# Kernel tuning notes

Hardware: AMD Instinct MI355X
Metric: run time of the kernel (lower is better)

Reference implementation:

```python
import jax, jax.numpy as jnp
import numpy as np

NHEAD = 16
EPS_ATTN = 1e-6
EPS_LN = 1e-5


def _layer_norm(x, g, b):
    mu = jnp.mean(x, -1, keepdims=True)
    var = jnp.mean((x - mu) ** 2, -1, keepdims=True)
    return (x - mu) * jax.lax.rsqrt(var + EPS_LN) * g + b


def _run_layer(x, S_prev, z_prev, lp, m):
    # x: (B,E); S_prev: (B,H,D,D); z_prev: (B,H,D,1); m: (B,1,1) or None
    qkv_w, qkv_b, out_w, out_b, n1g, n1b, n2g, n2b, f1w, f1b, f2w, f2b = lp
    B, E = x.shape
    H = NHEAD
    D = E // H
    qkv = x @ qkv_w.T + qkv_b
    q, k, v = [t.reshape(B, H, D) for t in jnp.split(qkv, 3, -1)]
    q = jax.nn.elu(q) + 1.0
    k = jax.nn.elu(k) + 1.0
    if m is not None:
        k = k * m
        v = v * m
    S_new = S_prev + jnp.einsum('bhd,bhm->bhdm', k, v)
    z_new = z_prev + k[..., None]
    num = jnp.einsum('bhd,bhdm->bhm', q, S_new)
    den = jnp.einsum('bhd,bhd->bh', q, z_new[..., 0])[..., None]
    attn = (num / (den + EPS_ATTN)).reshape(B, E)
    x = _layer_norm(x + attn @ out_w.T + out_b, n1g, n1b)
    h = jax.nn.relu(x @ f1w.T + f1b) @ f2w.T + f2b
    x = _layer_norm(x + h, n2g, n2b)
    return x, S_new, z_new


def _scan_layers(x_t, Ss, zs, params, m):
    # params: tuple of arrays each with leading layer dim L
    def body(x, xs):
        lp, S, z = xs
        x, S, z = _run_layer(x, S, z, lp, m)
        return x, (S, z)
    x_out, (Ss_new, zs_new) = jax.lax.scan(body, x_t, (params, Ss, zs))
    return x_out, Ss_new, zs_new


def _forward(x, lengths, out_lengths, emb_w, emb_b, enc_p, dec_p, fc_p):
    B, Slen, _ = x.shape
    E = emb_w.shape[0]
    H = NHEAD
    D = E // H
    L = enc_p[0].shape[0]
    h = x @ emb_w.T + emb_b
    # sinusoidal positional encoding
    pos = jnp.arange(Slen, dtype=h.dtype)[:, None]
    div = jnp.exp(jnp.arange(0, E, 2, dtype=h.dtype) * (-np.log(10000.0) / E))
    pe = jnp.zeros((Slen, E), h.dtype)
    pe = pe.at[:, 0::2].set(jnp.sin(pos * div)).at[:, 1::2].set(jnp.cos(pos * div))
    h = h + pe[None]
    mask = (jnp.arange(Slen)[None, :] < lengths[:, None]).astype(h.dtype)  # (B,S)
    Ss0 = jnp.zeros((L, B, H, D, D), h.dtype)
    zs0 = jnp.zeros((L, B, H, D, 1), h.dtype)

    def enc_step(carry, inp):
        Ss, zs, _ = carry
        x_t, m_t = inp
        x_out, Ss, zs = _scan_layers(x_t, Ss, zs, enc_p, m_t[:, None, None])
        return (Ss, zs, x_out), None

    (Ss, zs, x_last), _ = jax.lax.scan(
        enc_step, (Ss0, zs0, jnp.zeros((B, E), h.dtype)),
        (h.transpose(1, 0, 2), mask.T))

    fc1_w, fc1_b, fc2_w, fc2_b = fc_p

    def dec_step(carry, _):
        xd, Ss, zs = carry
        xd, Ss, zs = _scan_layers(xd, Ss, zs, dec_p, None)
        out = jax.nn.relu(xd @ fc1_w.T + fc1_b) @ fc2_w.T + fc2_b
        return (xd, Ss, zs), out

    _, outs = jax.lax.scan(dec_step, (x_last, Ss, zs), None, length=out_lengths)
    return outs.transpose(1, 0, 2)  # (B, out_lengths, num_classes)


def setup_inputs() -> dict:
    key = jax.random.key(0)
    B, S, IN, E, L, C, TOUT = 4, 256, 256, 1024, 4, 1000, 32
    ks = iter(jax.random.split(key, 64))

    def w(shape, s=0.02):
        return jax.random.normal(next(ks), shape, jnp.float32) * s

    d = {}
    d['x'] = jax.random.normal(next(ks), (B, S, IN), jnp.float32)
    d['lengths'] = jax.random.randint(next(ks), (B,), 1, S + 1)
    d['out_lengths'] = TOUT
    d['emb_w'] = w((E, IN))
    d['emb_b'] = jnp.zeros((E,), jnp.float32)
    for pre in ('enc', 'dec'):
        d[f'{pre}_qkv_w'] = w((L, 3 * E, E))
        d[f'{pre}_qkv_b'] = jnp.zeros((L, 3 * E), jnp.float32)
        d[f'{pre}_out_w'] = w((L, E, E))
        d[f'{pre}_out_b'] = jnp.zeros((L, E), jnp.float32)
        d[f'{pre}_n1g'] = jnp.ones((L, E), jnp.float32)
        d[f'{pre}_n1b'] = jnp.zeros((L, E), jnp.float32)
        d[f'{pre}_n2g'] = jnp.ones((L, E), jnp.float32)
        d[f'{pre}_n2b'] = jnp.zeros((L, E), jnp.float32)
        d[f'{pre}_f1w'] = w((L, E, E))  # dim_feedforward == hidden_size
        d[f'{pre}_f1b'] = jnp.zeros((L, E), jnp.float32)
        d[f'{pre}_f2w'] = w((L, E, E))
        d[f'{pre}_f2b'] = jnp.zeros((L, E), jnp.float32)
    d['fc1_w'] = w((E, E))
    d['fc1_b'] = jnp.zeros((E,), jnp.float32)
    d['fc2_w'] = w((C, E))
    d['fc2_b'] = jnp.zeros((C,), jnp.float32)
    return d


def reference(x, lengths, out_lengths, emb_w, emb_b,
              enc_qkv_w, enc_qkv_b, enc_out_w, enc_out_b, enc_n1g, enc_n1b,
              enc_n2g, enc_n2b, enc_f1w, enc_f1b, enc_f2w, enc_f2b,
              dec_qkv_w, dec_qkv_b, dec_out_w, dec_out_b, dec_n1g, dec_n1b,
              dec_n2g, dec_n2b, dec_f1w, dec_f1b, dec_f2w, dec_f2b,
              fc1_w, fc1_b, fc2_w, fc2_b):
    enc_p = (enc_qkv_w, enc_qkv_b, enc_out_w, enc_out_b, enc_n1g, enc_n1b,
             enc_n2g, enc_n2b, enc_f1w, enc_f1b, enc_f2w, enc_f2b)
    dec_p = (dec_qkv_w, dec_qkv_b, dec_out_w, dec_out_b, dec_n1g, dec_n1b,
             dec_n2g, dec_n2b, dec_f1w, dec_f1b, dec_f2w, dec_f2b)
    fc_p = (fc1_w, fc1_b, fc2_w, fc2_b)
    return _forward(x, lengths, out_lengths, emb_w, emb_b, enc_p, dec_p, fc_p)
```

## Files before the change

### kernel.cpp

```cpp
#include <hip/hip_runtime.h>
#include <hip/hip_bf16.h>
#include <cstdint>


#define EP_NONE     0
#define EP_PE       1
#define EP_QKV      2
#define EP_RELU     3
#define EP_RES      4

typedef __attribute__((ext_vector_type(8))) short bf8v;
typedef __attribute__((ext_vector_type(8))) unsigned short us8;
typedef __attribute__((ext_vector_type(4))) float f4_t;

__device__ __forceinline__ float bf2f(unsigned short s) {
    union { unsigned u; float f; } t; t.u = ((unsigned)s) << 16; return t.f;
}
__device__ __forceinline__ unsigned short f2bf(float f) {
    union { float f; unsigned u; } t; t.f = f;
    unsigned u = t.u;
    unsigned r = u + 0x7FFFu + ((u >> 16) & 1u);
    return (unsigned short)(r >> 16);
}
__device__ __forceinline__ float ldS(const void* p, size_t i, bool b) {
    return b ? bf2f(((const unsigned short*)p)[i]) : ((const float*)p)[i];
}
__device__ __forceinline__ void ld4d(const void* p, size_t i, bool b, float o[4]) {
    if (b) {
        ushort4 v = *(const ushort4*)((const unsigned short*)p + i);
        o[0] = bf2f(v.x); o[1] = bf2f(v.y); o[2] = bf2f(v.z); o[3] = bf2f(v.w);
    } else {
        float4 v = *(const float4*)((const float*)p + i);
        o[0] = v.x; o[1] = v.y; o[2] = v.z; o[3] = v.w;
    }
}
__device__ __forceinline__ void stS(void* p, size_t i, bool b, float v) {
    if (b) ((unsigned short*)p)[i] = f2bf(v);
    else   ((float*)p)[i] = v;
}

__device__ __forceinline__ void split_store(unsigned short* hp, unsigned short* lp,
                                            const float fv[8]) {
    us8 h, l;
#pragma unroll
    for (int i = 0; i < 8; ++i) {
        unsigned short hh = f2bf(fv[i]);
        h[i] = (short)hh;
        l[i] = f2bf(fv[i] - bf2f(hh));
    }
    *(us8*)hp = h;
    *(us8*)lp = l;
}

__global__ void detect_k(const unsigned* __restrict__ ones,
                         const int* __restrict__ lens, int* __restrict__ flag)
{
    if (threadIdx.x == 0 && blockIdx.x == 0) {
        flag[0] = (ones[0] == 0x3F803F80u) ? 1 : 0;
        flag[1] = (lens[1] == 0 && lens[3] == 0) ? 1 : 0;
    }
}

template <int EPI>
__global__ __launch_bounds__(256) void mgemm_k(
    const void* __restrict__ A, int a_ext, int t0, int chb,
    const void* __restrict__ W, size_t woff,
    const void* __restrict__ bias, size_t boff,
    const float* __restrict__ res, float* __restrict__ C,
    int M, int N, int K,
    const int* __restrict__ lengths, const int* __restrict__ flag)
{
    (void)M;
    const bool ebf = flag[0] != 0;
    const bool abf = ebf && (a_ext != 0);
    __shared__ __align__(16) unsigned short Ah[64][40];
    __shared__ __align__(16) unsigned short Al[64][40];
    __shared__ __align__(16) unsigned short Bh[64][40];
    __shared__ __align__(16) unsigned short Bl[64][40];

    const int tid = threadIdx.x;
    const int n0 = blockIdx.x << 6, m0 = blockIdx.y << 6;
    const int chm = (1 << chb) - 1;

    const int srow = tid >> 2;
    const int sc0 = (tid & 3) << 3;
    const int lrowA = m0 + srow;
    const size_t arow = a_ext ? ((size_t)(lrowA >> chb) * 256 + t0 + (lrowA & chm))
                              : (size_t)lrowA;
    const size_t abase = arow * (size_t)K + sc0;
    const size_t wbase = woff + (size_t)(n0 + srow) * K + sc0;

    const int lane = tid & 63;
    const int wv4 = tid >> 6;
    const int wm = (wv4 >> 1) << 5;
    const int wn = (wv4 & 1) << 5;
    const int fr = lane & 15;
    const int fk = (lane >> 4) << 3;

    f4_t a00 = {}, a01 = {}, a10 = {}, a11 = {};

    for (int k0 = 0; k0 < K; k0 += 32) {
        if (abf) {
            const unsigned short* ap = (const unsigned short*)A + abase + k0;
            *(us8*)&Ah[srow][sc0] = *(const us8*)ap;
            us8 z = {};
            *(us8*)&Al[srow][sc0] = z;
        } else {
            const float* ap = (const float*)A + abase + k0;
            float4 f0 = *(const float4*)ap;
            float4 f1 = *(const float4*)(ap + 4);
            float fv[8] = {f0.x, f0.y, f0.z, f0.w, f1.x, f1.y, f1.z, f1.w};
            split_store(&Ah[srow][sc0], &Al[srow][sc0], fv);
        }
        if (ebf) {
            const unsigned short* wp = (const unsigned short*)W + wbase + k0;
            *(us8*)&Bh[srow][sc0] = *(const us8*)wp;
        } else {
            const float* wp = (const float*)W + wbase + k0;
            float4 f0 = *(const float4*)wp;
            float4 f1 = *(const float4*)(wp + 4);
            float fv[8] = {f0.x, f0.y, f0.z, f0.w, f1.x, f1.y, f1.z, f1.w};
            split_store(&Bh[srow][sc0], &Bl[srow][sc0], fv);
        }
        __syncthreads();

        bf8v ah0 = *(const bf8v*)&Ah[wm + fr][fk];
        bf8v ah1 = *(const bf8v*)&Ah[wm + 16 + fr][fk];
        bf8v bh0 = *(const bf8v*)&Bh[wn + fr][fk];
        bf8v bh1 = *(const bf8v*)&Bh[wn + 16 + fr][fk];
        a00 = __builtin_amdgcn_mfma_f32_16x16x32_bf16(ah0, bh0, a00, 0, 0, 0);
        a01 = __builtin_amdgcn_mfma_f32_16x16x32_bf16(ah0, bh1, a01, 0, 0, 0);
        a10 = __builtin_amdgcn_mfma_f32_16x16x32_bf16(ah1, bh0, a10, 0, 0, 0);
        a11 = __builtin_amdgcn_mfma_f32_16x16x32_bf16(ah1, bh1, a11, 0, 0, 0);
        if (!abf) {
            bf8v al0 = *(const bf8v*)&Al[wm + fr][fk];
            bf8v al1 = *(const bf8v*)&Al[wm + 16 + fr][fk];
            a00 = __builtin_amdgcn_mfma_f32_16x16x32_bf16(al0, bh0, a00, 0, 0, 0);
            a01 = __builtin_amdgcn_mfma_f32_16x16x32_bf16(al0, bh1, a01, 0, 0, 0);
            a10 = __builtin_amdgcn_mfma_f32_16x16x32_bf16(al1, bh0, a10, 0, 0, 0);
            a11 = __builtin_amdgcn_mfma_f32_16x16x32_bf16(al1, bh1, a11, 0, 0, 0);
        }
        if (!ebf) {
            bf8v bl0 = *(const bf8v*)&Bl[wn + fr][fk];
            bf8v bl1 = *(const bf8v*)&Bl[wn + 16 + fr][fk];
            a00 = __builtin_amdgcn_mfma_f32_16x16x32_bf16(ah0, bl0, a00, 0, 0, 0);
            a01 = __builtin_amdgcn_mfma_f32_16x16x32_bf16(ah0, bl1, a01, 0, 0, 0);
            a10 = __builtin_amdgcn_mfma_f32_16x16x32_bf16(ah1, bl0, a10, 0, 0, 0);
            a11 = __builtin_amdgcn_mfma_f32_16x16x32_bf16(ah1, bl1, a11, 0, 0, 0);
        }
        __syncthreads();
    }

    f4_t accs[2][2] = {{a00, a01}, {a10, a11}};
    const int rb = m0 + wm + ((lane >> 4) << 2);
    const int cb = n0 + wn + fr;
#pragma unroll
    for (int i = 0; i < 2; ++i) {
#pragma unroll
        for (int e = 0; e < 4; ++e) {
            const int r = rb + i * 16 + e;
#pragma unroll
            for (int j = 0; j < 2; ++j) {
                const int c = cb + j * 16;
                float v = accs[i][j][e] + ldS(bias, boff + c, ebf);
                if constexpr (EPI == EP_PE) {
                    int t = t0 + (r & chm);
                    float freq = expf((float)(c & ~1) * (-9.210340371976184f / 1024.0f));
                    float ang = (float)t * freq;
                    v += (c & 1) ? cosf(ang) : sinf(ang);
                } else if constexpr (EPI == EP_QKV) {
                    if (c < 2048)
                        v = v > 0.f ? v + 1.f : expf(v);
                    if (c >= 1024) {
                        int bb = r >> chb, t = t0 + (r & chm);
                        int len = lengths[flag[1] ? (bb << 1) : bb];
                        if (t >= len) v = 0.f;
                    }
                } else if constexpr (EPI == EP_RELU) {
                    v = fmaxf(v, 0.f);
                } else if constexpr (EPI == EP_RES) {
                    v += res[(size_t)r * N + c];
                }
                C[(size_t)r * N + c] = v;
            }
        }
    }
}

__global__ __launch_bounds__(64) void enc_attn_k(
    const float* __restrict__ qkvc, float* __restrict__ attnc,
    float* __restrict__ Sst, float* __restrict__ zst, int first, int CH)
{
    const int bid = blockIdx.x;
    const int mg = bid & 3, h = (bid >> 2) & 15, b = bid >> 6;
    const int bh = b * 16 + h;
    const int tid = threadIdx.x;
    const int ml = tid & 15, d4 = tid >> 4, db = d4 << 4;
    const int m = (mg << 4) + ml;

    float Sa[16], za[16];
    if (first) {
#pragma unroll
        for (int j = 0; j < 16; ++j) { Sa[j] = 0.f; za[j] = 0.f; }
    } else {
#pragma unroll
        for (int j = 0; j < 16; ++j) {
            Sa[j] = Sst[(size_t)bh * 4096 + (size_t)(db + j) * 64 + m];
            za[j] = zst[(size_t)bh * 64 + db + j];
        }
    }

    __shared__ float ks[32][64];
    __shared__ float qs[32][64];
    __shared__ float vs[32][16];

    for (int s = 0; s < CH; s += 32) {
        __syncthreads();
        for (int r = 0; r < 32; ++r) {
            const float* p = qkvc + (size_t)(b * CH + s + r) * 3072 + (h << 6);
            qs[r][tid] = p[tid];
            ks[r][tid] = p[1024 + tid];
        }
        for (int i = tid; i < 512; i += 64) {
            int r = i >> 4, c = i & 15;
            vs[r][c] = qkvc[(size_t)(b * CH + s + r) * 3072 + 2048 + (h << 6) + (mg << 4) + c];
        }
        __syncthreads();

        for (int tt = 0; tt < 32; ++tt) {
            float v = vs[tt][ml];
            const float4* k4 = (const float4*)&ks[tt][db];
            const float4* q4 = (const float4*)&qs[tt][db];
            float pn = 0.f, pd = 0.f;
#pragma unroll
            for (int j = 0; j < 4; ++j) {
                float4 kk = k4[j], qq = q4[j];
                Sa[4*j+0] += kk.x * v; za[4*j+0] += kk.x;
                Sa[4*j+1] += kk.y * v; za[4*j+1] += kk.y;
                Sa[4*j+2] += kk.z * v; za[4*j+2] += kk.z;
                Sa[4*j+3] += kk.w * v; za[4*j+3] += kk.w;
                pn += qq.x*Sa[4*j+0] + qq.y*Sa[4*j+1] + qq.z*Sa[4*j+2] + qq.w*Sa[4*j+3];
                pd += qq.x*za[4*j+0] + qq.y*za[4*j+1] + qq.z*za[4*j+2] + qq.w*za[4*j+3];
            }
            pn += __shfl_xor(pn, 16); pd += __shfl_xor(pd, 16);
            pn += __shfl_xor(pn, 32); pd += __shfl_xor(pd, 32);
            if (d4 == 0)
                attnc[(size_t)(b * CH + s + tt) * 1024 + (h << 6) + m] = pn / (pd + 1e-6f);
        }
    }

#pragma unroll
    for (int j = 0; j < 16; ++j)
        Sst[(size_t)bh * 4096 + (size_t)(db + j) * 64 + m] = Sa[j];
    if (ml == 0) {
#pragma unroll
        for (int j = 0; j < 16; ++j)
            zst[(size_t)bh * 64 + db + j] = za[j];
    }
}

__global__ __launch_bounds__(256) void ln_k(
    float* __restrict__ Y, const void* __restrict__ g, size_t goff,
    const void* __restrict__ b, size_t boff, const int* __restrict__ flag)
{
    const bool ebf = flag[0] != 0;
    __shared__ float red[256];
    const int row = blockIdx.x, tid = threadIdx.x;
    float4* y4 = (float4*)(Y + (size_t)row * 1024);
    float4 x = y4[tid];
    red[tid] = x.x + x.y + x.z + x.w;
    __syncthreads();
    for (int o = 128; o > 0; o >>= 1) {
        if (tid < o) red[tid] += red[tid + o];
        __syncthreads();
    }
    float mu = red[0] * (1.0f / 1024.0f);
    __syncthreads();
    float dx = x.x - mu, dy = x.y - mu, dz = x.z - mu, dw = x.w - mu;
    red[tid] = dx * dx + dy * dy + dz * dz + dw * dw;
    __syncthreads();
    for (int o = 128; o > 0; o >>= 1) {
        if (tid < o) red[tid] += red[tid + o];
        __syncthreads();
    }
    float rs = rsqrtf(red[0] * (1.0f / 1024.0f) + 1e-5f);
    float gv[4], bv[4];
    ld4d(g, goff + (size_t)tid * 4, ebf, gv);
    ld4d(b, boff + (size_t)tid * 4, ebf, bv);
    float4 o;
    o.x = dx * rs * gv[0] + bv[0];
    o.y = dy * rs * gv[1] + bv[1];
    o.z = dz * rs * gv[2] + bv[2];
    o.w = dw * rs * gv[3] + bv[3];
    y4[tid] = o;
}

template <int EPI, bool XN, int RES, bool ODYN>
__global__ __launch_bounds__(256) void sgemm2_k(
    const float* __restrict__ x,
    const void* __restrict__ lxg, size_t lxgo,
    const void* __restrict__ lxb, size_t lxbo,
    const float* __restrict__ res,
    const void* __restrict__ lrg, size_t lrgo,
    const void* __restrict__ lrb, size_t lrbo,
    const void* __restrict__ W, size_t woff,
    const void* __restrict__ bias, size_t boff,
    void* __restrict__ C, int N, int K, int ldc, int coff,
    const int* __restrict__ flag)
{
    const bool ebf = flag[0] != 0;
    const int wv = threadIdx.x >> 6, lane = threadIdx.x & 63;
    __shared__ float sxm[4], sxr[4], srm[4], srr[4];

    if (XN) {
        const float4* xr = (const float4*)(x + (size_t)wv * K);
        float s = 0.f, q = 0.f;
        for (int i = lane; i < (K >> 2); i += 64) {
            float4 v = xr[i];
            s += v.x + v.y + v.z + v.w;
            q += v.x*v.x + v.y*v.y + v.z*v.z + v.w*v.w;
        }
        for (int o2 = 32; o2; o2 >>= 1) { s += __shfl_xor(s, o2); q += __shfl_xor(q, o2); }
        if (lane == 0) {
            float mu = s / (float)K;
            sxm[wv] = mu;
            sxr[wv] = rsqrtf(q / (float)K - mu * mu + 1e-5f);
        }
    }
    if (RES == 2) {
        const float4* rr = (const float4*)(res + (size_t)wv * N);
        float s = 0.f, q = 0.f;
        for (int i = lane; i < (N >> 2); i += 64) {
            float4 v = rr[i];
            s += v.x + v.y + v.z + v.w;
            q += v.x*v.x + v.y*v.y + v.z*v.z + v.w*v.w;
        }
        for (int o2 = 32; o2; o2 >>= 1) { s += __shfl_xor(s, o2); q += __shfl_xor(q, o2); }
        if (lane == 0) {
            float mu = s / (float)N;
            srm[wv] = mu;
            srr[wv] = rsqrtf(q / (float)N - mu * mu + 1e-5f);
        }
    }
    if (XN || RES == 2) __syncthreads();

    const int n = blockIdx.x * 4 + wv;
    const size_t wbase = woff + (size_t)n * K;
    const float4* x0 = (const float4*)(x);
    const float4* x1 = (const float4*)(x + K);
    const float4* x2 = (const float4*)(x + 2 * K);
    const float4* x3 = (const float4*)(x + 3 * K);
    float m0=0,r0=1,m1=0,r1=1,m2=0,r2=1,m3=0,r3=1;
    if (XN) {
        m0 = sxm[0]; r0 = sxr[0]; m1 = sxm[1]; r1 = sxr[1];
        m2 = sxm[2]; r2 = sxr[2]; m3 = sxm[3]; r3 = sxr[3];
    }
    float a0 = 0.f, a1 = 0.f, a2 = 0.f, a3 = 0.f;
    for (int i = lane; i < (K >> 2); i += 64) {
        float w[4];
        ld4d(W, wbase + (size_t)i * 4, ebf, w);
        float g[4], be[4];
        if (XN) {
            ld4d(lxg, lxgo + (size_t)i * 4, ebf, g);
            ld4d(lxb, lxbo + (size_t)i * 4, ebf, be);
        }
        float4 v;
#define ROWACC(XP, ACC, MU, RS)                                               \
        v = XP[i];                                                            \
        if (XN) {                                                             \
            ACC += ((v.x - MU) * RS * g[0] + be[0]) * w[0]                    \
                 + ((v.y - MU) * RS * g[1] + be[1]) * w[1]                    \
                 + ((v.z - MU) * RS * g[2] + be[2]) * w[2]                    \
                 + ((v.w - MU) * RS * g[3] + be[3]) * w[3];                   \
        } else {                                                              \
            ACC += v.x * w[0] + v.y * w[1] + v.z * w[2] + v.w * w[3];         \
        }
        ROWACC(x0, a0, m0, r0)
        ROWACC(x1, a1, m1, r1)
        ROWACC(x2, a2, m2, r2)
        ROWACC(x3, a3, m3, r3)
#undef ROWACC
    }
    for (int o2 = 32; o2; o2 >>= 1) {
        a0 += __shfl_down(a0, o2);
        a1 += __shfl_down(a1, o2);
        a2 += __shfl_down(a2, o2);
        a3 += __shfl_down(a3, o2);
    }
    if (lane == 0) {
        float bn = ldS(bias, boff + n, ebf);
        float v[4] = {a0 + bn, a1 + bn, a2 + bn, a3 + bn};
        float rg = 0.f, rb = 0.f;
        if (RES == 2) { rg = ldS(lrg, lrgo + n, ebf); rb = ldS(lrb, lrbo + n, ebf); }
#pragma unroll
        for (int b2 = 0; b2 < 4; ++b2) {
            if constexpr (RES == 1) {
                v[b2] += res[(size_t)b2 * N + n];
            } else if constexpr (RES == 2) {
                v[b2] += (res[(size_t)b2 * N + n] - srm[b2]) * srr[b2] * rg + rb;
            }
            if constexpr (EPI == EP_QKV) {
                if (n < 2048) v[b2] = v[b2] > 0.f ? v[b2] + 1.f : expf(v[b2]);
            } else if constexpr (EPI == EP_RELU) {
                v[b2] = fmaxf(v[b2], 0.f);
            }
            size_t idx = (size_t)coff + (size_t)b2 * ldc + n;
            if constexpr (ODYN) stS(C, idx, ebf, v[b2]);
            else                ((float*)C)[idx] = v[b2];
        }
    }
}

__global__ __launch_bounds__(64) void dec_attn_k(
    const float* __restrict__ qkv, float* __restrict__ Sst,
    float* __restrict__ zst, float* __restrict__ attn)
{
    const int bh = blockIdx.x;
    const int b = bh >> 4, h = bh & 15;
    const int lane = threadIdx.x;
    const float* base = qkv + (size_t)b * 3072 + (h << 6);
    float q = base[lane];
    float k = base[1024 + lane];
    float v = base[2048 + lane];
    __shared__ float kq[128];
    kq[lane] = k;
    kq[64 + lane] = q;
    float* zp = zst + (size_t)bh * 64;
    float zn = zp[lane] + k;
    zp[lane] = zn;
    float p = q * zn;
    for (int off = 32; off; off >>= 1) p += __shfl_xor(p, off);
    float den = p + 1e-6f;
    __syncthreads();
    float* Sp = Sst + (size_t)bh * 4096;
    float num = 0.f;
#pragma unroll 8
    for (int d = 0; d < 64; ++d) {
        float s = Sp[d * 64 + lane] + kq[d] * v;
        Sp[d * 64 + lane] = s;
        num += kq[64 + d] * s;
    }
    attn[(size_t)b * 1024 + (h << 6) + lane] = num / den;
}

__global__ __launch_bounds__(256) void copy_last_k(
    const float* __restrict__ Xc, float* __restrict__ xd, int CH)
{
    int i = blockIdx.x * 256 + threadIdx.x;
    int b = i >> 10, e = i & 1023;
    xd[i] = Xc[(size_t)(b * CH + CH - 1) * 1024 + e];
}

extern "C" void kernel_launch(void* const* d_in, const int* in_sizes, int n_in,
                              void* d_out, int out_size, void* d_ws, size_t ws_size,
                              hipStream_t stream)
{
    (void)n_in; (void)out_size;
    constexpr int E = 1024, B = 4, L = 4, TOUT = 32, NC = 1000;

    const int CH  = (ws_size >= (size_t)30 * 1024 * 1024) ? 256 : 32;
    const int chb = (CH == 256) ? 8 : 5;
    const int NCH = 256 / CH;
    const int MC  = B * CH;

    const int o = (in_sizes[2] == 1) ? 0 : -1;

    const void* x_in = d_in[0];
    const int*  lens = (const int*)d_in[1];
    const void* emb_w = d_in[3 + o];
    const void* emb_b = d_in[4 + o];
    const void* e_qkv_w = d_in[5 + o];  const void* e_qkv_b = d_in[6 + o];
    const void* e_out_w = d_in[7 + o];  const void* e_out_b = d_in[8 + o];
    const void* e_n1g = d_in[9 + o];    const void* e_n1b = d_in[10 + o];
    const void* e_n2g = d_in[11 + o];   const void* e_n2b = d_in[12 + o];
    const void* e_f1w = d_in[13 + o];   const void* e_f1b = d_in[14 + o];
    const void* e_f2w = d_in[15 + o];   const void* e_f2b = d_in[16 + o];
    const void* d_qkv_w = d_in[17 + o]; const void* d_qkv_b = d_in[18 + o];
    const void* d_out_w = d_in[19 + o]; const void* d_out_b = d_in[20 + o];
    const void* d_n1g = d_in[21 + o];   const void* d_n1b = d_in[22 + o];
    const void* d_n2g = d_in[23 + o];   const void* d_n2b = d_in[24 + o];
    const void* d_f1w = d_in[25 + o];   const void* d_f1b = d_in[26 + o];
    const void* d_f2w = d_in[27 + o];   const void* d_f2b = d_in[28 + o];
    const void* fc1_w = d_in[29 + o];   const void* fc1_b = d_in[30 + o];
    const void* fc2_w = d_in[31 + o];   const void* fc2_b = d_in[32 + o];

    float* wsf   = (float*)d_ws;
    int*   flag  = (int*)d_ws;
    float* u     = wsf + 64;
    float* t1    = u + B * E;
    float* qkvd  = t1 + B * E;
    float* attnd = qkvd + B * 3 * E;
    float* hfd   = attnd + B * E;
    float* Xc    = hfd + B * E;
    float* Yc    = Xc + (size_t)MC * E;
    float* attnc = Yc + (size_t)MC * E;
    float* qkvc  = attnc + (size_t)MC * E;
    float* zs    = qkvc + (size_t)MC * 3 * E;
    float* Ss    = zs + (size_t)L * B * 16 * 64;
    float* Hc    = qkvc;

    const size_t SstL = (size_t)B * 16 * 64 * 64;
    const size_t zstL = (size_t)B * 16 * 64;

    detect_k<<<1, 64, 0, stream>>>((const unsigned*)e_n1g, lens, flag);

    for (int c = 0; c < NCH; ++c) {
        const int t0 = c * CH;
        mgemm_k<EP_PE><<<dim3(E / 64, MC / 64), 256, 0, stream>>>(
            x_in, 1, t0, chb, emb_w, 0, emb_b, 0, nullptr, Xc,
            MC, E, 256, lens, flag);

        for (int l = 0; l < L; ++l) {
            const size_t qw_o = (size_t)l * 3 * E * E, qb_o = (size_t)l * 3 * E;
            const size_t ow_o = (size_t)l * E * E,     ob_o = (size_t)l * E;
            const size_t fw_o = (size_t)l * E * E,     fb_o = (size_t)l * E;
            const size_t g_o  = (size_t)l * E;

            mgemm_k<EP_QKV><<<dim3(3 * E / 64, MC / 64), 256, 0, stream>>>(
                Xc, 0, t0, chb, e_qkv_w, qw_o, e_qkv_b, qb_o, nullptr, qkvc,
                MC, 3 * E, E, lens, flag);
            enc_attn_k<<<B * 16 * 4, 64, 0, stream>>>(
                qkvc, attnc, Ss + l * SstL, zs + l * zstL, c == 0 ? 1 : 0, CH);
            mgemm_k<EP_RES><<<dim3(E / 64, MC / 64), 256, 0, stream>>>(
                attnc, 0, t0, chb, e_out_w, ow_o, e_out_b, ob_o, Xc, Yc,
                MC, E, E, lens, flag);
            ln_k<<<MC, 256, 0, stream>>>(Yc, e_n1g, g_o, e_n1b, g_o, flag);
            mgemm_k<EP_RELU><<<dim3(E / 64, MC / 64), 256, 0, stream>>>(
                Yc, 0, t0, chb, e_f1w, fw_o, e_f1b, fb_o, nullptr, Hc,
                MC, E, E, lens, flag);
            mgemm_k<EP_RES><<<dim3(E / 64, MC / 64), 256, 0, stream>>>(
                Hc, 0, t0, chb, e_f2w, fw_o, e_f2b, fb_o, Yc, Xc,
                MC, E, E, lens, flag);
            ln_k<<<MC, 256, 0, stream>>>(Xc, e_n2g, g_o, e_n2b, g_o, flag);
        }
    }

    copy_last_k<<<16, 256, 0, stream>>>(Xc, u, CH);

    for (int t = 0; t < TOUT; ++t) {
        for (int l = 0; l < L; ++l) {
            const size_t qw_o = (size_t)l * 3 * E * E, qb_o = (size_t)l * 3 * E;
            const size_t ow_o = (size_t)l * E * E,     ob_o = (size_t)l * E;
            const size_t fw_o = (size_t)l * E * E,     fb_o = (size_t)l * E;
            const size_t g_o  = (size_t)l * E;
            const size_t pg_o = (size_t)((l == 0) ? 3 : (l - 1)) * E;

            if (t == 0 && l == 0)
                sgemm2_k<EP_QKV, false, 0, false><<<3 * E / 4, 256, 0, stream>>>(
                    u, nullptr, 0, nullptr, 0, nullptr, nullptr, 0, nullptr, 0,
                    d_qkv_w, qw_o, d_qkv_b, qb_o, qkvd, 3 * E, E, 3 * E, 0, flag);
            else
                sgemm2_k<EP_QKV, true, 0, false><<<3 * E / 4, 256, 0, stream>>>(
                    u, d_n2g, pg_o, d_n2b, pg_o, nullptr, nullptr, 0, nullptr, 0,
                    d_qkv_w, qw_o, d_qkv_b, qb_o, qkvd, 3 * E, E, 3 * E, 0, flag);

            dec_attn_k<<<B * 16, 64, 0, stream>>>(
                qkvd, Ss + l * SstL, zs + l * zstL, attnd);

            if (t == 0 && l == 0)
                sgemm2_k<EP_NONE, false, 1, false><<<E / 4, 256, 0, stream>>>(
                    attnd, nullptr, 0, nullptr, 0, u, nullptr, 0, nullptr, 0,
                    d_out_w, ow_o, d_out_b, ob_o, t1, E, E, E, 0, flag);
            else
                sgemm2_k<EP_NONE, false, 2, false><<<E / 4, 256, 0, stream>>>(
                    attnd, nullptr, 0, nullptr, 0, u, d_n2g, pg_o, d_n2b, pg_o,
                    d_out_w, ow_o, d_out_b, ob_o, t1, E, E, E, 0, flag);

            sgemm2_k<EP_RELU, true, 0, false><<<E / 4, 256, 0, stream>>>(
                t1, d_n1g, g_o, d_n1b, g_o, nullptr, nullptr, 0, nullptr, 0,
                d_f1w, fw_o, d_f1b, fb_o, hfd, E, E, E, 0, flag);

            sgemm2_k<EP_NONE, false, 2, false><<<E / 4, 256, 0, stream>>>(
                hfd, nullptr, 0, nullptr, 0, t1, d_n1g, g_o, d_n1b, g_o,
                d_f2w, fw_o, d_f2b, fb_o, u, E, E, E, 0, flag);
        }
        sgemm2_k<EP_RELU, true, 0, false><<<E / 4, 256, 0, stream>>>(
            u, d_n2g, (size_t)3 * E, d_n2b, (size_t)3 * E,
            nullptr, nullptr, 0, nullptr, 0,
            fc1_w, 0, fc1_b, 0, hfd, E, E, E, 0, flag);
        sgemm2_k<EP_NONE, false, 0, true><<<NC / 4, 256, 0, stream>>>(
            hfd, nullptr, 0, nullptr, 0, nullptr, nullptr, 0, nullptr, 0,
            fc2_w, 0, fc2_b, 0, d_out, NC, E, TOUT * NC, t * NC, flag);
    }
}
```

Before: 5.739 ms.

## Fuse decoder step loop into one persistent kernel with grid barriers

Replaces roughly seven hundred small decoder launches (GEMV stages and per-head attention) with a single persistent kernel of 128 workgroups. Each wave strides over output rows, and a hierarchical atomic grid barrier separates the stages. The attention step now broadcasts q and k with shuffles instead of shared memory, and the barrier counters are reset in copy_last_k. The aim is to remove per-launch overhead and launch gaps. In exchange it keeps only 128 workgroups busy during the bandwidth-bound GEMVs, adds spin-barrier latency at every stage, and relies on all workgroups being co-resident.

After: 14.13 ms. 2.46x slower.

```diff
diff --git a/kernel.cpp b/kernel.cpp
--- a/kernel.cpp
+++ b/kernel.cpp
@@ -8,6 +8,9 @@
 #define EP_QKV      2
 #define EP_RELU     3
 #define EP_RES      4
+
+#define DEC_NWG     128
+#define DEC_NWAVE   (DEC_NWG * 4)
 
 typedef __attribute__((ext_vector_type(8))) short bf8v;
 typedef __attribute__((ext_vector_type(8))) unsigned short us8;
@@ -295,8 +298,32 @@
     y4[tid] = o;
 }
 
+
+__device__ __forceinline__ void gbar(unsigned* bar, unsigned idx)
+{
+    __syncthreads();
+    if (threadIdx.x == 0) {
+        const unsigned wpl = DEC_NWG / 4;
+        unsigned* leaf = bar + (blockIdx.x & 3);
+        unsigned lv = __hip_atomic_fetch_add(leaf, 1u, __ATOMIC_ACQ_REL,
+                                             __HIP_MEMORY_SCOPE_AGENT);
+        if (lv == idx * wpl + (wpl - 1)) {
+            unsigned rv = __hip_atomic_fetch_add(bar + 4, 1u, __ATOMIC_ACQ_REL,
+                                                 __HIP_MEMORY_SCOPE_AGENT);
+            if (rv == idx * 4 + 3)
+                __hip_atomic_store(bar + 5, idx + 1, __ATOMIC_RELEASE,
+                                   __HIP_MEMORY_SCOPE_AGENT);
+        }
+        while (__hip_atomic_load(bar + 5, __ATOMIC_RELAXED,
+                                 __HIP_MEMORY_SCOPE_AGENT) < idx + 1)
+            __builtin_amdgcn_s_sleep(4);
+        __threadfence();
+    }
+    __syncthreads();
+}
+
 template <int EPI, bool XN, int RES, bool ODYN>
-__global__ __launch_bounds__(256) void sgemm2_k(
+__device__ __forceinline__ void dstage(
     const float* __restrict__ x,
     const void* __restrict__ lxg, size_t lxgo,
     const void* __restrict__ lxb, size_t lxbo,
@@ -305,18 +332,17 @@
     const void* __restrict__ lrb, size_t lrbo,
     const void* __restrict__ W, size_t woff,
     const void* __restrict__ bias, size_t boff,
-    void* __restrict__ C, int N, int K, int ldc, int coff,
-    const int* __restrict__ flag)
-{
-    const bool ebf = flag[0] != 0;
-    const int wv = threadIdx.x >> 6, lane = threadIdx.x & 63;
-    __shared__ float sxm[4], sxr[4], srm[4], srr[4];
-
-    if (XN) {
+    void* __restrict__ C, int N, int ldc, int coff,
+    bool ebf, int wv, int lane,
+    float* sxm, float* sxr, float* srm, float* srr)
+{
+    constexpr int K = 1024;
+    if constexpr (XN) {
         const float4* xr = (const float4*)(x + (size_t)wv * K);
         float s = 0.f, q = 0.f;
-        for (int i = lane; i < (K >> 2); i += 64) {
-            float4 v = xr[i];
+#pragma unroll
+        for (int ii = 0; ii < 4; ++ii) {
+            float4 v = xr[lane + ii * 64];
             s += v.x + v.y + v.z + v.w;
             q += v.x*v.x + v.y*v.y + v.z*v.z + v.w*v.w;
         }
@@ -327,125 +353,205 @@
             sxr[wv] = rsqrtf(q / (float)K - mu * mu + 1e-5f);
         }
     }
-    if (RES == 2) {
-        const float4* rr = (const float4*)(res + (size_t)wv * N);
+    if constexpr (RES == 2) {
+        const float4* rr = (const float4*)(res + (size_t)wv * 1024);
         float s = 0.f, q = 0.f;
-        for (int i = lane; i < (N >> 2); i += 64) {
-            float4 v = rr[i];
+#pragma unroll
+        for (int ii = 0; ii < 4; ++ii) {
+            float4 v = rr[lane + ii * 64];
             s += v.x + v.y + v.z + v.w;
             q += v.x*v.x + v.y*v.y + v.z*v.z + v.w*v.w;
         }
         for (int o2 = 32; o2; o2 >>= 1) { s += __shfl_xor(s, o2); q += __shfl_xor(q, o2); }
         if (lane == 0) {
-            float mu = s / (float)N;
+            float mu = s / 1024.0f;
             srm[wv] = mu;
-            srr[wv] = rsqrtf(q / (float)N - mu * mu + 1e-5f);
-        }
-    }
-    if (XN || RES == 2) __syncthreads();
-
-    const int n = blockIdx.x * 4 + wv;
-    const size_t wbase = woff + (size_t)n * K;
+            srr[wv] = rsqrtf(q / 1024.0f - mu * mu + 1e-5f);
+        }
+    }
+    if constexpr (XN || RES == 2) __syncthreads();
+
+    float m0=0,r0=1,m1=0,r1=1,m2=0,r2=1,m3=0,r3=1;
+    if constexpr (XN) {
+        m0 = sxm[0]; r0 = sxr[0]; m1 = sxm[1]; r1 = sxr[1];
+        m2 = sxm[2]; r2 = sxr[2]; m3 = sxm[3]; r3 = sxr[3];
+    }
     const float4* x0 = (const float4*)(x);
     const float4* x1 = (const float4*)(x + K);
     const float4* x2 = (const float4*)(x + 2 * K);
     const float4* x3 = (const float4*)(x + 3 * K);
-    float m0=0,r0=1,m1=0,r1=1,m2=0,r2=1,m3=0,r3=1;
-    if (XN) {
-        m0 = sxm[0]; r0 = sxr[0]; m1 = sxm[1]; r1 = sxr[1];
-        m2 = sxm[2]; r2 = sxr[2]; m3 = sxm[3]; r3 = sxr[3];
-    }
-    float a0 = 0.f, a1 = 0.f, a2 = 0.f, a3 = 0.f;
-    for (int i = lane; i < (K >> 2); i += 64) {
-        float w[4];
-        ld4d(W, wbase + (size_t)i * 4, ebf, w);
-        float g[4], be[4];
-        if (XN) {
-            ld4d(lxg, lxgo + (size_t)i * 4, ebf, g);
-            ld4d(lxb, lxbo + (size_t)i * 4, ebf, be);
-        }
-        float4 v;
-#define ROWACC(XP, ACC, MU, RS)                                               \
-        v = XP[i];                                                            \
-        if (XN) {                                                             \
-            ACC += ((v.x - MU) * RS * g[0] + be[0]) * w[0]                    \
-                 + ((v.y - MU) * RS * g[1] + be[1]) * w[1]                    \
-                 + ((v.z - MU) * RS * g[2] + be[2]) * w[2]                    \
-                 + ((v.w - MU) * RS * g[3] + be[3]) * w[3];                   \
-        } else {                                                              \
-            ACC += v.x * w[0] + v.y * w[1] + v.z * w[2] + v.w * w[3];         \
-        }
-        ROWACC(x0, a0, m0, r0)
-        ROWACC(x1, a1, m1, r1)
-        ROWACC(x2, a2, m2, r2)
-        ROWACC(x3, a3, m3, r3)
-#undef ROWACC
-    }
-    for (int o2 = 32; o2; o2 >>= 1) {
-        a0 += __shfl_down(a0, o2);
-        a1 += __shfl_down(a1, o2);
-        a2 += __shfl_down(a2, o2);
-        a3 += __shfl_down(a3, o2);
-    }
-    if (lane == 0) {
-        float bn = ldS(bias, boff + n, ebf);
-        float v[4] = {a0 + bn, a1 + bn, a2 + bn, a3 + bn};
-        float rg = 0.f, rb = 0.f;
-        if (RES == 2) { rg = ldS(lrg, lrgo + n, ebf); rb = ldS(lrb, lrbo + n, ebf); }
-#pragma unroll
-        for (int b2 = 0; b2 < 4; ++b2) {
-            if constexpr (RES == 1) {
-                v[b2] += res[(size_t)b2 * N + n];
-            } else if constexpr (RES == 2) {
-                v[b2] += (res[(size_t)b2 * N + n] - srm[b2]) * srr[b2] * rg + rb;
+
+    for (int n = blockIdx.x * 4 + wv; n < N; n += DEC_NWAVE) {
+        const size_t wbase = woff + (size_t)n * K;
+        float a0 = 0.f, a1 = 0.f, a2 = 0.f, a3 = 0.f;
+#pragma unroll
+        for (int ii = 0; ii < 4; ++ii) {
+            const int i = lane + ii * 64;
+            float w[4];
+            ld4d(W, wbase + (size_t)i * 4, ebf, w);
+            float g[4], be[4];
+            if constexpr (XN) {
+                ld4d(lxg, lxgo + (size_t)i * 4, ebf, g);
+                ld4d(lxb, lxbo + (size_t)i * 4, ebf, be);
             }
-            if constexpr (EPI == EP_QKV) {
-                if (n < 2048) v[b2] = v[b2] > 0.f ? v[b2] + 1.f : expf(v[b2]);
-            } else if constexpr (EPI == EP_RELU) {
-                v[b2] = fmaxf(v[b2], 0.f);
+            float4 v;
+#define ROWACC2(XP, ACC, MU, RS)                                              \
+            v = XP[i];                                                        \
+            if constexpr (XN) {                                               \
+                ACC += ((v.x - MU) * RS * g[0] + be[0]) * w[0]                \
+                     + ((v.y - MU) * RS * g[1] + be[1]) * w[1]                \
+                     + ((v.z - MU) * RS * g[2] + be[2]) * w[2]                \
+                     + ((v.w - MU) * RS * g[3] + be[3]) * w[3];               \
+            } else {                                                          \
+                ACC += v.x * w[0] + v.y * w[1] + v.z * w[2] + v.w * w[3];     \
             }
-            size_t idx = (size_t)coff + (size_t)b2 * ldc + n;
-            if constexpr (ODYN) stS(C, idx, ebf, v[b2]);
-            else                ((float*)C)[idx] = v[b2];
-        }
-    }
-}
-
-__global__ __launch_bounds__(64) void dec_attn_k(
-    const float* __restrict__ qkv, float* __restrict__ Sst,
-    float* __restrict__ zst, float* __restrict__ attn)
-{
-    const int bh = blockIdx.x;
-    const int b = bh >> 4, h = bh & 15;
-    const int lane = threadIdx.x;
-    const float* base = qkv + (size_t)b * 3072 + (h << 6);
+            ROWACC2(x0, a0, m0, r0)
+            ROWACC2(x1, a1, m1, r1)
+            ROWACC2(x2, a2, m2, r2)
+            ROWACC2(x3, a3, m3, r3)
+#undef ROWACC2
+        }
+        for (int o2 = 32; o2; o2 >>= 1) {
+            a0 += __shfl_down(a0, o2);
+            a1 += __shfl_down(a1, o2);
+            a2 += __shfl_down(a2, o2);
+            a3 += __shfl_down(a3, o2);
+        }
+        if (lane == 0) {
+            float bn = ldS(bias, boff + n, ebf);
+            float v[4] = {a0 + bn, a1 + bn, a2 + bn, a3 + bn};
+            float rg = 0.f, rb = 0.f;
+            if constexpr (RES == 2) { rg = ldS(lrg, lrgo + n, ebf); rb = ldS(lrb, lrbo + n, ebf); }
+#pragma unroll
+            for (int b2 = 0; b2 < 4; ++b2) {
+                if constexpr (RES == 1) {
+                    v[b2] += res[(size_t)b2 * 1024 + n];
+                } else if constexpr (RES == 2) {
+                    v[b2] += (res[(size_t)b2 * 1024 + n] - srm[b2]) * srr[b2] * rg + rb;
+                }
+                if constexpr (EPI == EP_QKV) {
+                    if (n < 2048) v[b2] = v[b2] > 0.f ? v[b2] + 1.f : expf(v[b2]);
+                } else if constexpr (EPI == EP_RELU) {
+                    v[b2] = fmaxf(v[b2], 0.f);
+                }
+                size_t idx = (size_t)coff + (size_t)b2 * ldc + n;
+                if constexpr (ODYN) stS(C, idx, ebf, v[b2]);
+                else                ((float*)C)[idx] = v[b2];
+            }
+        }
+    }
+}
+
+__device__ __forceinline__ void dattn(
+    const float* __restrict__ qkvd, float* __restrict__ Sst,
+    float* __restrict__ zst, float* __restrict__ attnd, int wv, int lane)
+{
+    const int g = blockIdx.x;
+    if (g >= 64 || wv != 0) return;
+    const int b = g >> 4, h = g & 15;
+    const float* base = qkvd + (size_t)b * 3072 + (h << 6);
     float q = base[lane];
     float k = base[1024 + lane];
     float v = base[2048 + lane];
-    __shared__ float kq[128];
-    kq[lane] = k;
-    kq[64 + lane] = q;
-    float* zp = zst + (size_t)bh * 64;
+    float* zp = zst + (size_t)g * 64;
     float zn = zp[lane] + k;
     zp[lane] = zn;
     float p = q * zn;
     for (int off = 32; off; off >>= 1) p += __shfl_xor(p, off);
     float den = p + 1e-6f;
-    __syncthreads();
-    float* Sp = Sst + (size_t)bh * 4096;
+    float* Sp = Sst + (size_t)g * 4096;
     float num = 0.f;
 #pragma unroll 8
     for (int d = 0; d < 64; ++d) {
-        float s = Sp[d * 64 + lane] + kq[d] * v;
+        float kd = __shfl(k, d);
+        float qd = __shfl(q, d);
+        float s = Sp[d * 64 + lane] + kd * v;
         Sp[d * 64 + lane] = s;
-        num += kq[64 + d] * s;
-    }
-    attn[(size_t)b * 1024 + (h << 6) + lane] = num / den;
+        num += qd * s;
+    }
+    attnd[(size_t)b * 1024 + (h << 6) + lane] = num / den;
+}
+
+__global__ __launch_bounds__(256) void dec_pers_k(
+    const void* qkv_w, const void* qkv_b, const void* out_w, const void* out_b,
+    const void* n1g, const void* n1b, const void* n2g, const void* n2b,
+    const void* f1w, const void* f1b, const void* f2w, const void* f2b,
+    const void* fc1w, const void* fc1b, const void* fc2w, const void* fc2b,
+    float* u, float* t1, float* qkvd, float* attnd, float* hfd,
+    float* Ss, float* zs, void* outp, const int* flag, unsigned* bar)
+{
+    constexpr int E = 1024, L = 4, TOUT = 32, NC = 1000;
+    const bool ebf = flag[0] != 0;
+    const int wv = threadIdx.x >> 6, lane = threadIdx.x & 63;
+    __shared__ float sxm[4], sxr[4], srm[4], srr[4];
+    const size_t SstL = (size_t)4 * 16 * 64 * 64;
+    const size_t zstL = (size_t)4 * 16 * 64;
+    unsigned bidx = 0;
+
+    for (int t = 0; t < TOUT; ++t) {
+        for (int l = 0; l < L; ++l) {
+            const size_t qw_o = (size_t)l * 3 * E * E, qb_o = (size_t)l * 3 * E;
+            const size_t ow_o = (size_t)l * E * E,     ob_o = (size_t)l * E;
+            const size_t fw_o = (size_t)l * E * E,     fb_o = (size_t)l * E;
+            const size_t g_o  = (size_t)l * E;
+            const size_t pg_o = (size_t)((l == 0) ? 3 : (l - 1)) * E;
+
+            if (t == 0 && l == 0)
+                dstage<EP_QKV, false, 0, false>(
+                    u, nullptr, 0, nullptr, 0, nullptr, nullptr, 0, nullptr, 0,
+                    qkv_w, qw_o, qkv_b, qb_o, qkvd, 3 * E, 3 * E, 0,
+                    ebf, wv, lane, sxm, sxr, srm, srr);
+            else
+                dstage<EP_QKV, true, 0, false>(
+                    u, n2g, pg_o, n2b, pg_o, nullptr, nullptr, 0, nullptr, 0,
+                    qkv_w, qw_o, qkv_b, qb_o, qkvd, 3 * E, 3 * E, 0,
+                    ebf, wv, lane, sxm, sxr, srm, srr);
+            gbar(bar, bidx++);
+
+            dattn(qkvd, Ss + l * SstL, zs + l * zstL, attnd, wv, lane);
+            gbar(bar, bidx++);
+
+            if (t == 0 && l == 0)
+                dstage<EP_NONE, false, 1, false>(
+                    attnd, nullptr, 0, nullptr, 0, u, nullptr, 0, nullptr, 0,
+                    out_w, ow_o, out_b, ob_o, t1, E, E, 0,
+                    ebf, wv, lane, sxm, sxr, srm, srr);
+            else
+                dstage<EP_NONE, false, 2, false>(
+                    attnd, nullptr, 0, nullptr, 0, u, n2g, pg_o, n2b, pg_o,
+                    out_w, ow_o, out_b, ob_o, t1, E, E, 0,
+                    ebf, wv, lane, sxm, sxr, srm, srr);
+            gbar(bar, bidx++);
+
+            dstage<EP_RELU, true, 0, false>(
+                t1, n1g, g_o, n1b, g_o, nullptr, nullptr, 0, nullptr, 0,
+                f1w, fw_o, f1b, fb_o, hfd, E, E, 0,
+                ebf, wv, lane, sxm, sxr, srm, srr);
+            gbar(bar, bidx++);
+
+            dstage<EP_NONE, false, 2, false>(
+                hfd, nullptr, 0, nullptr, 0, t1, n1g, g_o, n1b, g_o,
+                f2w, fw_o, f2b, fb_o, u, E, E, 0,
+                ebf, wv, lane, sxm, sxr, srm, srr);
+            gbar(bar, bidx++);
+        }
+        dstage<EP_RELU, true, 0, false>(
+            u, n2g, (size_t)3 * E, n2b, (size_t)3 * E, nullptr, nullptr, 0, nullptr, 0,
+            fc1w, 0, fc1b, 0, hfd, E, E, 0,
+            ebf, wv, lane, sxm, sxr, srm, srr);
+        gbar(bar, bidx++);
+        dstage<EP_NONE, false, 0, true>(
+            hfd, nullptr, 0, nullptr, 0, nullptr, nullptr, 0, nullptr, 0,
+            fc2w, 0, fc2b, 0, outp, NC, TOUT * NC, t * NC,
+            ebf, wv, lane, sxm, sxr, srm, srr);
+    }
 }
 
 __global__ __launch_bounds__(256) void copy_last_k(
-    const float* __restrict__ Xc, float* __restrict__ xd, int CH)
-{
+    const float* __restrict__ Xc, float* __restrict__ xd, int CH,
+    unsigned* __restrict__ bar)
+{
+    if (blockIdx.x == 0 && threadIdx.x < 8) bar[threadIdx.x] = 0u;
     int i = blockIdx.x * 256 + threadIdx.x;
     int b = i >> 10, e = i & 1023;
     xd[i] = Xc[(size_t)(b * CH + CH - 1) * 1024 + e];
@@ -456,7 +562,7 @@
                               hipStream_t stream)
 {
     (void)n_in; (void)out_size;
-    constexpr int E = 1024, B = 4, L = 4, TOUT = 32, NC = 1000;
+    constexpr int E = 1024, B = 4, L = 4;
 
     const int CH  = (ws_size >= (size_t)30 * 1024 * 1024) ? 256 : 32;
     const int chb = (CH == 256) ? 8 : 5;
@@ -486,6 +592,7 @@
 
     float* wsf   = (float*)d_ws;
     int*   flag  = (int*)d_ws;
+    unsigned* bar = (unsigned*)d_ws + 16;
     float* u     = wsf + 64;
     float* t1    = u + B * E;
     float* qkvd  = t1 + B * E;
@@ -535,51 +642,13 @@
         }
     }
 
-    copy_last_k<<<16, 256, 0, stream>>>(Xc, u, CH);
-
-    for (int t = 0; t < TOUT; ++t) {
-        for (int l = 0; l < L; ++l) {
-            const size_t qw_o = (size_t)l * 3 * E * E, qb_o = (size_t)l * 3 * E;
-            const size_t ow_o = (size_t)l * E * E,     ob_o = (size_t)l * E;
-            const size_t fw_o = (size_t)l * E * E,     fb_o = (size_t)l * E;
-            const size_t g_o  = (size_t)l * E;
-            const size_t pg_o = (size_t)((l == 0) ? 3 : (l - 1)) * E;
-
-            if (t == 0 && l == 0)
-                sgemm2_k<EP_QKV, false, 0, false><<<3 * E / 4, 256, 0, stream>>>(
-                    u, nullptr, 0, nullptr, 0, nullptr, nullptr, 0, nullptr, 0,
-                    d_qkv_w, qw_o, d_qkv_b, qb_o, qkvd, 3 * E, E, 3 * E, 0, flag);
-            else
-                sgemm2_k<EP_QKV, true, 0, false><<<3 * E / 4, 256, 0, stream>>>(
-                    u, d_n2g, pg_o, d_n2b, pg_o, nullptr, nullptr, 0, nullptr, 0,
-                    d_qkv_w, qw_o, d_qkv_b, qb_o, qkvd, 3 * E, E, 3 * E, 0, flag);
-
-            dec_attn_k<<<B * 16, 64, 0, stream>>>(
-                qkvd, Ss + l * SstL, zs + l * zstL, attnd);
-
-            if (t == 0 && l == 0)
-                sgemm2_k<EP_NONE, false, 1, false><<<E / 4, 256, 0, stream>>>(
-                    attnd, nullptr, 0, nullptr, 0, u, nullptr, 0, nullptr, 0,
-                    d_out_w, ow_o, d_out_b, ob_o, t1, E, E, E, 0, flag);
-            else
-                sgemm2_k<EP_NONE, false, 2, false><<<E / 4, 256, 0, stream>>>(
-                    attnd, nullptr, 0, nullptr, 0, u, d_n2g, pg_o, d_n2b, pg_o,
-                    d_out_w, ow_o, d_out_b, ob_o, t1, E, E, E, 0, flag);
-
-            sgemm2_k<EP_RELU, true, 0, false><<<E / 4, 256, 0, stream>>>(
-                t1, d_n1g, g_o, d_n1b, g_o, nullptr, nullptr, 0, nullptr, 0,
-                d_f1w, fw_o, d_f1b, fb_o, hfd, E, E, E, 0, flag);
-
-            sgemm2_k<EP_NONE, false, 2, false><<<E / 4, 256, 0, stream>>>(
-                hfd, nullptr, 0, nullptr, 0, t1, d_n1g, g_o, d_n1b, g_o,
-                d_f2w, fw_o, d_f2b, fb_o, u, E, E, E, 0, flag);
-        }
-        sgemm2_k<EP_RELU, true, 0, false><<<E / 4, 256, 0, stream>>>(
-            u, d_n2g, (size_t)3 * E, d_n2b, (size_t)3 * E,
-            nullptr, nullptr, 0, nullptr, 0,
-            fc1_w, 0, fc1_b, 0, hfd, E, E, E, 0, flag);
-        sgemm2_k<EP_NONE, false, 0, true><<<NC / 4, 256, 0, stream>>>(
-            hfd, nullptr, 0, nullptr, 0, nullptr, nullptr, 0, nullptr, 0,
-            fc2_w, 0, fc2_b, 0, d_out, NC, E, TOUT * NC, t * NC, flag);
-    }
-}
+    copy_last_k<<<16, 256, 0, stream>>>(Xc, u, CH, bar);
+
+    dec_pers_k<<<DEC_NWG, 256, 0, stream>>>(
+        d_qkv_w, d_qkv_b, d_out_w, d_out_b,
+        d_n1g, d_n1b, d_n2g, d_n2b,
+        d_f1w, d_f1b, d_f2w, d_f2b,
+        fc1_w, fc1_b, fc2_w, fc2_b,
+        u, t1, qkvd, attnd, hfd,
+        Ss, zs, d_out, flag, bar);
+}
```
